# Kernel tuning notes

Hardware: AMD Instinct MI355X
Metric: run time of the kernel (lower is better)

## Reference

```python
import jax, jax.numpy as jnp
import numpy as np

B, C, H, W = 8, 256, 64, 64
CM = C // 4          # mask channels (theta/phi out) = 64
CI = C - CM          # img channels = 192
EPS = 1e-5


def setup_inputs() -> dict:
    key = jax.random.key(0)
    ks = jax.random.split(key, 12)
    return {
        "x": jax.random.normal(ks[0], (B, C, H, W), dtype=jnp.float32),
        "g_w": jax.random.normal(ks[1], (C, C), dtype=jnp.float32) * 0.05,
        "g_b": jax.random.normal(ks[2], (C,), dtype=jnp.float32) * 0.01,
        "theta_w": jax.random.normal(ks[3], (CM, CM), dtype=jnp.float32) * 0.1,
        "theta_b": jax.random.normal(ks[4], (CM,), dtype=jnp.float32) * 0.01,
        "phi_w": jax.random.normal(ks[5], (CM, CI), dtype=jnp.float32) * 0.06,
        "phi_b": jax.random.normal(ks[6], (CM,), dtype=jnp.float32) * 0.01,
        "W_w": jax.random.normal(ks[7], (C, C), dtype=jnp.float32) * 0.05,
        "W_b": jax.random.normal(ks[8], (C,), dtype=jnp.float32) * 0.01,
        "bn_gamma": jax.random.normal(ks[9], (C,), dtype=jnp.float32) * 0.1 + 1.0,
        "bn_beta": jax.random.normal(ks[10], (C,), dtype=jnp.float32) * 0.01,
        "bn_mean": jax.random.normal(ks[11], (C,), dtype=jnp.float32) * 0.1,
        "bn_var": jnp.ones((C,), dtype=jnp.float32),
    }


def _conv1x1(t, w, b):
    # [B,Cin,H,W] x [Cout,Cin] -> [B,Cout,H,W]
    return jnp.einsum('bchw,oc->bohw', t, w) + b[None, :, None, None]


def _maxpool2(t):
    b, c, h, w = t.shape
    return t.reshape(b, c, h // 2, 2, w // 2, 2).max(axis=(3, 5))


def reference(x, g_w, g_b, theta_w, theta_b, phi_w, phi_b, W_w, W_b,
              bn_gamma, bn_beta, bn_mean, bn_var):
    b, c, h, w = x.shape
    ci = c // 4
    mask_ch = x[:, :ci]          # [B, C/4, H, W]
    img_ch = x[:, ci:]           # [B, 3C/4, H, W]

    # g: conv1x1 then 2x2 maxpool -> [B, C, N'] -> [B, N', C]
    g_x = _maxpool2(_conv1x1(x, g_w, g_b)).reshape(b, c, -1).transpose(0, 2, 1)
    # theta: conv1x1 on mask -> [B, N, C/4]
    theta_x = _conv1x1(mask_ch, theta_w, theta_b).reshape(b, ci, -1).transpose(0, 2, 1)
    # phi: conv1x1 on img then pool -> [B, C/4, N']
    phi_x = _maxpool2(_conv1x1(img_ch, phi_w, phi_b)).reshape(b, ci, -1)

    f = jnp.einsum('bnc,bcm->bnm', theta_x, phi_x)     # [B, N, N']
    f_div_C = jax.nn.softmax(f, axis=-1)
    y = jnp.einsum('bnm,bmc->bnc', f_div_C, g_x)       # [B, N, C]
    y = y.transpose(0, 2, 1).reshape(b, c, h, w)

    W_y = _conv1x1(y, W_w, W_b)
    # BatchNorm (inference form with running stats)
    inv = jax.lax.rsqrt(bn_var + EPS)
    W_y = (W_y - bn_mean[None, :, None, None]) * (inv * bn_gamma)[None, :, None, None] \
          + bn_beta[None, :, None, None]
    return W_y + x
```

## Files before the change

kernel.cpp:

```cpp
#include <hip/hip_runtime.h>
#include <hip/hip_bf16.h>

typedef __hip_bfloat16 bf16;
typedef unsigned short ushort;
typedef unsigned int uint;
typedef __attribute__((ext_vector_type(8))) short short8;
typedef __attribute__((ext_vector_type(4))) float f32x4;

#define Bn 8
#define Cn 256
#define Nn 4096
#define Mn 1024
#define EPSf 1e-5f

__device__ __forceinline__ float b2f(const bf16 v){ return __bfloat162float(v); }
__device__ __forceinline__ ushort f2bu(float f){
  uint u = __float_as_uint(f);
  return (ushort)((u + 0x7FFFu + ((u >> 16) & 1u)) >> 16);
}

__global__ __launch_bounds__(256) void transpose_kernel(
    const float* __restrict__ x, bf16* __restrict__ xT)
{
  __shared__ float xs[64][65];
  const int t = threadIdx.x;
  const int p0 = blockIdx.x*64, c0 = blockIdx.y*64, b = blockIdx.z;
  #pragma unroll
  for (int i = 0; i < 16; ++i) {
    int idx = t + i*256; int cl = idx >> 6, pl = idx & 63;
    xs[cl][pl] = x[((long)(b*Cn) + c0 + cl)*Nn + p0 + pl];
  }
  __syncthreads();
  ushort* xTu = (ushort*)xT;
  #pragma unroll
  for (int i = 0; i < 8; ++i) {
    int idx = t + i*256; int pl = idx >> 5, cp = idx & 31;
    uint u = (uint)f2bu(xs[cp*2][pl]) | ((uint)f2bu(xs[cp*2+1][pl]) << 16);
    *(uint*)(xTu + ((long)(b*Nn) + p0 + pl)*Cn + c0 + cp*2) = u;
  }
}

__global__ __launch_bounds__(256) void wcomb_kernel(
    const float* __restrict__ tw, const float* __restrict__ tb,
    const float* __restrict__ pw, const float* __restrict__ pb,
    const float* __restrict__ gw, const float* __restrict__ gb,
    bf16* __restrict__ Wcomb, float* __restrict__ bcomb)
{
  const int r = blockIdx.x, c = threadIdx.x;
  float v;
  if (r < 64)        v = (c < 64)  ? tw[r*64 + c]            : 0.f;
  else if (r < 128)  v = (c >= 64) ? pw[(r-64)*192 + (c-64)] : 0.f;
  else               v = gw[(r-128)*256 + c];
  Wcomb[r*256 + c] = __float2bfloat16(v);
  if (c == 0)
    bcomb[r] = (r < 64) ? tb[r] : (r < 128) ? pb[r-64] : gb[r-128];
}

__global__ __launch_bounds__(256) void gemm384_kernel(
    const bf16* __restrict__ xT, const bf16* __restrict__ Wcomb,
    const float* __restrict__ bcomb, bf16* __restrict__ Q,
    bf16* __restrict__ K, bf16* __restrict__ Vt)
{
  __shared__ union {
    struct { ushort As[128*40]; ushort Bs[128*40]; } g;
    float Pb[2][128][33];
  } sm;
  const int t = threadIdx.x;
  const int px = blockIdx.x, o0 = blockIdx.y*128, b = blockIdx.z;
  const int p0 = px*128;
  const int lane = t & 63, w = t >> 6;
  const int ql = lane & 15, quad = lane >> 4;
  const int wm = (w & 1)*64, wn = (w >> 1)*64;
  const ushort* xTu = (const ushort*)xT;
  const ushort* Wu  = (const ushort*)Wcomb;

  f32x4 acc[4][4];
  #pragma unroll
  for (int i = 0; i < 4; ++i)
    #pragma unroll
    for (int j = 0; j < 4; ++j) acc[i][j] = (f32x4){0.f,0.f,0.f,0.f};

  for (int kc = 0; kc < 8; ++kc) {
    __syncthreads();
    #pragma unroll
    for (int i = 0; i < 2; ++i) {
      int idx = t + i*256; int r = idx >> 2, cq = idx & 3;
      *(uint4*)(sm.g.As + r*40 + cq*8) =
          *(const uint4*)(xTu + ((long)(b*Nn) + p0 + r)*Cn + kc*32 + cq*8);
      *(uint4*)(sm.g.Bs + r*40 + cq*8) =
          *(const uint4*)(Wu + (o0 + r)*Cn + kc*32 + cq*8);
    }
    __syncthreads();
    short8 aF[4], bF[4];
    #pragma unroll
    for (int mi = 0; mi < 4; ++mi)
      aF[mi] = *(const short8*)(sm.g.As + (wm + mi*16 + ql)*40 + quad*8);
    #pragma unroll
    for (int ni = 0; ni < 4; ++ni)
      bF[ni] = *(const short8*)(sm.g.Bs + (wn + ni*16 + ql)*40 + quad*8);
    #pragma unroll
    for (int mi = 0; mi < 4; ++mi)
      #pragma unroll
      for (int ni = 0; ni < 4; ++ni)
        acc[mi][ni] = __builtin_amdgcn_mfma_f32_16x16x32_bf16(aF[mi], bF[ni], acc[mi][ni], 0, 0, 0);
  }
  float bias[4];
  #pragma unroll
  for (int ni = 0; ni < 4; ++ni) bias[ni] = bcomb[o0 + wn + ni*16 + ql];

  if (o0 == 0 && wn == 0) {
    #pragma unroll
    for (int mi = 0; mi < 4; ++mi)
      #pragma unroll
      for (int ni = 0; ni < 4; ++ni)
        #pragma unroll
        for (int r = 0; r < 4; ++r) {
          int p = p0 + wm + mi*16 + quad*4 + r;
          Q[((long)(b*Nn) + p)*64 + ni*16 + ql] = __float2bfloat16(acc[mi][ni][r] + bias[ni]);
        }
  }
  __syncthreads();
  if (o0 != 0 || wn == 64) {
    int g = w & 1;
    #pragma unroll
    for (int mi = 0; mi < 4; ++mi)
      #pragma unroll
      for (int ni = 0; ni < 4; ++ni) {
        float a0 = acc[mi][ni][0] + bias[ni], a1 = acc[mi][ni][1] + bias[ni];
        float a2 = acc[mi][ni][2] + bias[ni], a3 = acc[mi][ni][3] + bias[ni];
        int o = wn + ni*16 + ql;
        int wp = mi*8 + quad*2;
        sm.Pb[g][o][wp]     = fmaxf(a0, a1);
        sm.Pb[g][o][wp + 1] = fmaxf(a2, a3);
      }
  }
  __syncthreads();
  if (o0 == 0) {
    int wp = t & 31, og = t >> 5;
    ushort kv[8];
    #pragma unroll
    for (int j = 0; j < 8; ++j) {
      int o = 64 + og*8 + j;
      kv[j] = f2bu(fmaxf(sm.Pb[0][o][wp], sm.Pb[1][o][wp]));
    }
    *(uint4*)((ushort*)K + ((long)(b*Mn) + px*32 + wp)*64 + og*8) = *(uint4*)kv;
  } else {
    int ol = t >> 1, wp0 = (t & 1)*16;
    ushort vv[16];
    #pragma unroll
    for (int j = 0; j < 16; ++j)
      vv[j] = f2bu(fmaxf(sm.Pb[0][ol][wp0 + j], sm.Pb[1][ol][wp0 + j]));
    ushort* dst = (ushort*)Vt + ((long)(b*Cn) + (o0 - 128) + ol)*Mn + px*32 + wp0;
    *(uint4*)dst       = *(uint4*)(vv);
    *(uint4*)(dst + 8) = *(uint4*)(vv + 8);
  }
}

__global__ __launch_bounds__(256) void attn_kernel(
    const bf16* __restrict__ Q, const bf16* __restrict__ K, const bf16* __restrict__ Vt,
    bf16* __restrict__ Y)
{
  __shared__ __align__(16) ushort Ks[64*72];
  __shared__ __align__(16) ushort Vs[256*72];
  __shared__ __align__(16) ushort Ps[64*72];
  __shared__ float a_sh[64];
  __shared__ float l_sh[64];

  const int t = threadIdx.x;
  const int b = blockIdx.y, q0 = blockIdx.x*64;
  const int lane = t & 63, w = t >> 6;
  const int ql = lane & 15, quad = lane >> 4;
  const int rql = w*16;
  const int pvr = (w & 1)*32;
  const int pvc = (w >> 1)*128;
  const ushort* Qu = (const ushort*)Q;
  const ushort* Ku = (const ushort*)K;
  const ushort* Vu = (const ushort*)Vt;

  short8 aQ0 = *(const short8*)(Qu + ((long)(b*Nn) + q0 + rql + ql)*64 + quad*8);
  short8 aQ1 = *(const short8*)(Qu + ((long)(b*Nn) + q0 + rql + ql)*64 + 32 + quad*8);

  float mrow[4], lrow[4];
  #pragma unroll
  for (int r = 0; r < 4; ++r) { mrow[r] = -3e38f; lrow[r] = 0.f; }

  f32x4 acc[2][8];
  #pragma unroll
  for (int mi = 0; mi < 2; ++mi)
    #pragma unroll
    for (int ci = 0; ci < 8; ++ci) acc[mi][ci] = (f32x4){0.f,0.f,0.f,0.f};

  for (int mt = 0; mt < 16; ++mt) {
    const int m0 = mt*64;
    __syncthreads();
    {
      int ch = t & 7, rr = t >> 3;
      #pragma unroll
      for (int i = 0; i < 2; ++i) {
        int row = rr + 32*i;
        *(uint4*)(Ks + row*72 + ch*8) =
            *(const uint4*)(Ku + ((long)(b*Mn) + m0 + row)*64 + ch*8);
      }
      #pragma unroll
      for (int p = 0; p < 8; ++p) {
        int n = rr + 32*p;
        *(uint4*)(Vs + n*72 + ch*8) =
            *(const uint4*)(Vu + ((long)(b*Cn) + n)*Mn + m0 + ch*8);
      }
    }
    __syncthreads();
    f32x4 s[4];
    #pragma unroll
    for (int ct = 0; ct < 4; ++ct) {
      short8 b0 = *(const short8*)(Ks + (ct*16 + ql)*72 + quad*8);
      short8 b1 = *(const short8*)(Ks + (ct*16 + ql)*72 + 32 + quad*8);
      s[ct] = (f32x4){0.f,0.f,0.f,0.f};
      s[ct] = __builtin_amdgcn_mfma_f32_16x16x32_bf16(aQ0, b0, s[ct], 0, 0, 0);
      s[ct] = __builtin_amdgcn_mfma_f32_16x16x32_bf16(aQ1, b1, s[ct], 0, 0, 0);
    }
    float alpha[4];
    #pragma unroll
    for (int r = 0; r < 4; ++r) {
      float mx = fmaxf(fmaxf(s[0][r], s[1][r]), fmaxf(s[2][r], s[3][r]));
      #pragma unroll
      for (int off = 1; off < 16; off <<= 1) mx = fmaxf(mx, __shfl_xor(mx, off, 64));
      float mn = fmaxf(mrow[r], mx);
      alpha[r] = __expf(mrow[r] - mn);
      mrow[r] = mn;
      float sum = 0.f;
      #pragma unroll
      for (int ct = 0; ct < 4; ++ct) { s[ct][r] = __expf(s[ct][r] - mn); sum += s[ct][r]; }
      #pragma unroll
      for (int off = 1; off < 16; off <<= 1) sum += __shfl_xor(sum, off, 64);
      lrow[r] = lrow[r]*alpha[r] + sum;
    }
    #pragma unroll
    for (int ct = 0; ct < 4; ++ct)
      #pragma unroll
      for (int r = 0; r < 4; ++r)
        Ps[(rql + quad*4 + r)*72 + ct*16 + ql] = f2bu(s[ct][r]);
    if (ql == 0) {
      #pragma unroll
      for (int r = 0; r < 4; ++r) a_sh[rql + quad*4 + r] = alpha[r];
    }
    __syncthreads();
    #pragma unroll
    for (int mi = 0; mi < 2; ++mi) {
      #pragma unroll
      for (int r = 0; r < 4; ++r) {
        float alv = a_sh[pvr + mi*16 + quad*4 + r];
        #pragma unroll
        for (int ci = 0; ci < 8; ++ci) acc[mi][ci][r] *= alv;
      }
    }
    short8 aP0[2], aP1[2];
    #pragma unroll
    for (int mi = 0; mi < 2; ++mi) {
      aP0[mi] = *(const short8*)(Ps + (pvr + mi*16 + ql)*72 + quad*8);
      aP1[mi] = *(const short8*)(Ps + (pvr + mi*16 + ql)*72 + 32 + quad*8);
    }
    #pragma unroll
    for (int ci = 0; ci < 8; ++ci) {
      short8 b0 = *(const short8*)(Vs + (pvc + ci*16 + ql)*72 + quad*8);
      short8 b1 = *(const short8*)(Vs + (pvc + ci*16 + ql)*72 + 32 + quad*8);
      #pragma unroll
      for (int mi = 0; mi < 2; ++mi) {
        acc[mi][ci] = __builtin_amdgcn_mfma_f32_16x16x32_bf16(aP0[mi], b0, acc[mi][ci], 0, 0, 0);
        acc[mi][ci] = __builtin_amdgcn_mfma_f32_16x16x32_bf16(aP1[mi], b1, acc[mi][ci], 0, 0, 0);
      }
    }
  }
  if (ql == 0) {
    #pragma unroll
    for (int r = 0; r < 4; ++r) l_sh[rql + quad*4 + r] = lrow[r];
  }
  __syncthreads();
  #pragma unroll
  for (int mi = 0; mi < 2; ++mi)
    #pragma unroll
    for (int r = 0; r < 4; ++r) {
      int row = pvr + mi*16 + quad*4 + r;
      float inv = 1.f / l_sh[row];
      #pragma unroll
      for (int ci = 0; ci < 8; ++ci)
        Y[((long)(b*Nn) + q0 + row)*256 + pvc + ci*16 + ql] = __float2bfloat16(acc[mi][ci][r]*inv);
    }
}

__global__ __launch_bounds__(256) void wconv_kernel(
    const bf16* __restrict__ Y, const float* __restrict__ Ww, const float* __restrict__ Wb,
    const float* __restrict__ gamma, const float* __restrict__ beta,
    const float* __restrict__ mean, const float* __restrict__ var,
    const float* __restrict__ x, float* __restrict__ out)
{
  __shared__ __align__(16) ushort As[128*40];
  __shared__ __align__(16) ushort Bs[128*40];
  __shared__ float ssc[128], ssh[128];
  const int t = threadIdx.x;
  const int n0 = blockIdx.x*128, o0 = blockIdx.y*128, b = blockIdx.z;
  const int lane = t & 63, w = t >> 6;
  const int ql = lane & 15, quad = lane >> 4;
  const int wm = (w & 1)*64, wn = (w >> 1)*64;
  const ushort* Yu = (const ushort*)Y;

  if (t < 128) {
    int o = o0 + t;
    float sc = gamma[o] * rsqrtf(var[o] + EPSf);
    ssc[t] = sc;
    ssh[t] = (Wb[o] - mean[o])*sc + beta[o];
  }

  f32x4 acc[4][4];
  #pragma unroll
  for (int i = 0; i < 4; ++i)
    #pragma unroll
    for (int j = 0; j < 4; ++j) acc[i][j] = (f32x4){0.f,0.f,0.f,0.f};

  for (int kc = 0; kc < 8; ++kc) {
    __syncthreads();
    #pragma unroll
    for (int i = 0; i < 4; ++i) {
      int idx = t + i*256; int r = idx >> 3, cq = idx & 7;
      float4 v = *(const float4*)(Ww + (o0 + r)*Cn + kc*32 + cq*4);
      uint lo = (uint)f2bu(v.x) | ((uint)f2bu(v.y) << 16);
      uint hi = (uint)f2bu(v.z) | ((uint)f2bu(v.w) << 16);
      *(uint2*)(As + r*40 + cq*4) = make_uint2(lo, hi);
    }
    #pragma unroll
    for (int i = 0; i < 2; ++i) {
      int idx = t + i*256; int r = idx >> 2, cq = idx & 3;
      *(uint4*)(Bs + r*40 + cq*8) =
          *(const uint4*)(Yu + ((long)(b*Nn) + n0 + r)*Cn + kc*32 + cq*8);
    }
    __syncthreads();
    short8 aF[4], bF[4];
    #pragma unroll
    for (int mi = 0; mi < 4; ++mi)
      aF[mi] = *(const short8*)(As + (wm + mi*16 + ql)*40 + quad*8);
    #pragma unroll
    for (int ni = 0; ni < 4; ++ni)
      bF[ni] = *(const short8*)(Bs + (wn + ni*16 + ql)*40 + quad*8);
    #pragma unroll
    for (int mi = 0; mi < 4; ++mi)
      #pragma unroll
      for (int ni = 0; ni < 4; ++ni)
        acc[mi][ni] = __builtin_amdgcn_mfma_f32_16x16x32_bf16(aF[mi], bF[ni], acc[mi][ni], 0, 0, 0);
  }
  #pragma unroll
  for (int mi = 0; mi < 4; ++mi)
    #pragma unroll
    for (int r = 0; r < 4; ++r) {
      int ol = wm + mi*16 + quad*4 + r;
      int o = o0 + ol;
      float sc = ssc[ol], sh = ssh[ol];
      #pragma unroll
      for (int ni = 0; ni < 4; ++ni) {
        int n = n0 + wn + ni*16 + ql;
        long gidx = ((long)(b*Cn + o))*Nn + n;
        out[gidx] = acc[mi][ni][r]*sc + sh + x[gidx];
      }
    }
}

extern "C" void kernel_launch(void* const* d_in, const int* in_sizes, int n_in,
                              void* d_out, int out_size, void* d_ws, size_t ws_size,
                              hipStream_t stream)
{
  const float* x       = (const float*)d_in[0];
  const float* g_w     = (const float*)d_in[1];
  const float* g_b     = (const float*)d_in[2];
  const float* theta_w = (const float*)d_in[3];
  const float* theta_b = (const float*)d_in[4];
  const float* phi_w   = (const float*)d_in[5];
  const float* phi_b   = (const float*)d_in[6];
  const float* W_w     = (const float*)d_in[7];
  const float* W_b     = (const float*)d_in[8];
  const float* bn_g    = (const float*)d_in[9];
  const float* bn_b    = (const float*)d_in[10];
  const float* bn_m    = (const float*)d_in[11];
  const float* bn_v    = (const float*)d_in[12];
  float* out = (float*)d_out;

  bf16* wsb = (bf16*)d_ws;
  bf16* xT    = wsb;
  bf16* Y     = wsb;
  bf16* Q     = wsb + 8388608;
  bf16* K     = wsb + 10485760;
  bf16* Vt    = wsb + 11010048;
  bf16* Wcomb = wsb + 13107200;
  float* bcomb = (float*)(wsb + 13205504);

  transpose_kernel<<<dim3(64, 4, Bn), 256, 0, stream>>>(x, xT);
  wcomb_kernel<<<dim3(384), 256, 0, stream>>>(theta_w, theta_b, phi_w, phi_b, g_w, g_b, Wcomb, bcomb);
  gemm384_kernel<<<dim3(32, 3, Bn), 256, 0, stream>>>(xT, Wcomb, bcomb, Q, K, Vt);
  attn_kernel<<<dim3(64, Bn), 256, 0, stream>>>(Q, K, Vt, Y);
  wconv_kernel<<<dim3(32, 2, Bn), 256, 0, stream>>>(Y, W_w, W_b, bn_g, bn_b, bn_m, bn_v, x, out);
}
```

Baseline: 201.9 us.

## Precompute softmax row max in a first pass and drop online rescaling

The attention kernel now runs an extra pass over all K tiles, read straight from global memory, to compute the exact row maximum before the main loop. The main loop then drops the per-tile max reduction, the alpha rescaling of the accumulators and the a_sh shared array, and only accumulates unnormalised exp sums, which are reduced once at the end. The LDS row pitch also shrinks from 72 to 68 elements. That pitch gives 136-byte rows, so the 16-byte LDS vector accesses are no longer 16-byte aligned, which may split or slow them. The extra pass also recomputes the QK products once more.

Measured after the change: 216.6 us. 7.3% more time.

```diff
diff --git a/kernel.cpp b/kernel.cpp
--- a/kernel.cpp
+++ b/kernel.cpp
@@ -160,10 +160,9 @@
     const bf16* __restrict__ Q, const bf16* __restrict__ K, const bf16* __restrict__ Vt,
     bf16* __restrict__ Y)
 {
-  __shared__ __align__(16) ushort Ks[64*72];
-  __shared__ __align__(16) ushort Vs[256*72];
-  __shared__ __align__(16) ushort Ps[64*72];
-  __shared__ float a_sh[64];
+  __shared__ __align__(16) ushort Ks[64*68];
+  __shared__ __align__(16) ushort Vs[256*68];
+  __shared__ __align__(16) ushort Ps[64*68];
   __shared__ float l_sh[64];
 
   const int t = threadIdx.x;
@@ -177,12 +176,35 @@
   const ushort* Ku = (const ushort*)K;
   const ushort* Vu = (const ushort*)Vt;
 
-  short8 aQ0 = *(const short8*)(Qu + ((long)(b*Nn) + q0 + rql + ql)*64 + quad*8);
-  short8 aQ1 = *(const short8*)(Qu + ((long)(b*Nn) + q0 + rql + ql)*64 + 32 + quad*8);
-
-  float mrow[4], lrow[4];
-  #pragma unroll
-  for (int r = 0; r < 4; ++r) { mrow[r] = -3e38f; lrow[r] = 0.f; }
+  const long qrow = (long)(b*Nn) + q0 + rql + ql;
+  short8 aQ0 = *(const short8*)(Qu + qrow*64 + quad*8);
+  short8 aQ1 = *(const short8*)(Qu + qrow*64 + 32 + quad*8);
+
+  float mrow[4];
+  #pragma unroll
+  for (int r = 0; r < 4; ++r) mrow[r] = -3e38f;
+  for (int mt = 0; mt < 16; ++mt) {
+    const ushort* kb = Ku + ((long)(b*Mn) + mt*64)*64;
+    #pragma unroll
+    for (int ct = 0; ct < 4; ++ct) {
+      short8 b0 = *(const short8*)(kb + (ct*16 + ql)*64 + quad*8);
+      short8 b1 = *(const short8*)(kb + (ct*16 + ql)*64 + 32 + quad*8);
+      f32x4 s = (f32x4){0.f,0.f,0.f,0.f};
+      s = __builtin_amdgcn_mfma_f32_16x16x32_bf16(aQ0, b0, s, 0, 0, 0);
+      s = __builtin_amdgcn_mfma_f32_16x16x32_bf16(aQ1, b1, s, 0, 0, 0);
+      #pragma unroll
+      for (int r = 0; r < 4; ++r) mrow[r] = fmaxf(mrow[r], s[r]);
+    }
+  }
+  #pragma unroll
+  for (int r = 0; r < 4; ++r)
+    #pragma unroll
+    for (int off = 1; off < 16; off <<= 1)
+      mrow[r] = fmaxf(mrow[r], __shfl_xor(mrow[r], off, 64));
+
+  float lrow[4];
+  #pragma unroll
+  for (int r = 0; r < 4; ++r) lrow[r] = 0.f;
 
   f32x4 acc[2][8];
   #pragma unroll
@@ -198,13 +220,13 @@
       #pragma unroll
       for (int i = 0; i < 2; ++i) {
         int row = rr + 32*i;
-        *(uint4*)(Ks + row*72 + ch*8) =
+        *(uint4*)(Ks + row*68 + ch*8) =
             *(const uint4*)(Ku + ((long)(b*Mn) + m0 + row)*64 + ch*8);
       }
       #pragma unroll
       for (int p = 0; p < 8; ++p) {
         int n = rr + 32*p;
-        *(uint4*)(Vs + n*72 + ch*8) =
+        *(uint4*)(Vs + n*68 + ch*8) =
             *(const uint4*)(Vu + ((long)(b*Cn) + n)*Mn + m0 + ch*8);
       }
     }
@@ -212,57 +234,31 @@
     f32x4 s[4];
     #pragma unroll
     for (int ct = 0; ct < 4; ++ct) {
-      short8 b0 = *(const short8*)(Ks + (ct*16 + ql)*72 + quad*8);
-      short8 b1 = *(const short8*)(Ks + (ct*16 + ql)*72 + 32 + quad*8);
+      short8 b0 = *(const short8*)(Ks + (ct*16 + ql)*68 + quad*8);
+      short8 b1 = *(const short8*)(Ks + (ct*16 + ql)*68 + 32 + quad*8);
       s[ct] = (f32x4){0.f,0.f,0.f,0.f};
       s[ct] = __builtin_amdgcn_mfma_f32_16x16x32_bf16(aQ0, b0, s[ct], 0, 0, 0);
       s[ct] = __builtin_amdgcn_mfma_f32_16x16x32_bf16(aQ1, b1, s[ct], 0, 0, 0);
     }
-    float alpha[4];
-    #pragma unroll
-    for (int r = 0; r < 4; ++r) {
-      float mx = fmaxf(fmaxf(s[0][r], s[1][r]), fmaxf(s[2][r], s[3][r]));
-      #pragma unroll
-      for (int off = 1; off < 16; off <<= 1) mx = fmaxf(mx, __shfl_xor(mx, off, 64));
-      float mn = fmaxf(mrow[r], mx);
-      alpha[r] = __expf(mrow[r] - mn);
-      mrow[r] = mn;
-      float sum = 0.f;
-      #pragma unroll
-      for (int ct = 0; ct < 4; ++ct) { s[ct][r] = __expf(s[ct][r] - mn); sum += s[ct][r]; }
-      #pragma unroll
-      for (int off = 1; off < 16; off <<= 1) sum += __shfl_xor(sum, off, 64);
-      lrow[r] = lrow[r]*alpha[r] + sum;
-    }
     #pragma unroll
     for (int ct = 0; ct < 4; ++ct)
       #pragma unroll
-      for (int r = 0; r < 4; ++r)
-        Ps[(rql + quad*4 + r)*72 + ct*16 + ql] = f2bu(s[ct][r]);
-    if (ql == 0) {
-      #pragma unroll
-      for (int r = 0; r < 4; ++r) a_sh[rql + quad*4 + r] = alpha[r];
-    }
-    __syncthreads();
+      for (int r = 0; r < 4; ++r) {
+        float e = __expf(s[ct][r] - mrow[r]);
+        lrow[r] += e;
+        Ps[(rql + quad*4 + r)*68 + ct*16 + ql] = f2bu(e);
+      }
+    __syncthreads();
+    short8 aP0[2], aP1[2];
     #pragma unroll
     for (int mi = 0; mi < 2; ++mi) {
-      #pragma unroll
-      for (int r = 0; r < 4; ++r) {
-        float alv = a_sh[pvr + mi*16 + quad*4 + r];
-        #pragma unroll
-        for (int ci = 0; ci < 8; ++ci) acc[mi][ci][r] *= alv;
-      }
-    }
-    short8 aP0[2], aP1[2];
-    #pragma unroll
-    for (int mi = 0; mi < 2; ++mi) {
-      aP0[mi] = *(const short8*)(Ps + (pvr + mi*16 + ql)*72 + quad*8);
-      aP1[mi] = *(const short8*)(Ps + (pvr + mi*16 + ql)*72 + 32 + quad*8);
+      aP0[mi] = *(const short8*)(Ps + (pvr + mi*16 + ql)*68 + quad*8);
+      aP1[mi] = *(const short8*)(Ps + (pvr + mi*16 + ql)*68 + 32 + quad*8);
     }
     #pragma unroll
     for (int ci = 0; ci < 8; ++ci) {
-      short8 b0 = *(const short8*)(Vs + (pvc + ci*16 + ql)*72 + quad*8);
-      short8 b1 = *(const short8*)(Vs + (pvc + ci*16 + ql)*72 + 32 + quad*8);
+      short8 b0 = *(const short8*)(Vs + (pvc + ci*16 + ql)*68 + quad*8);
+      short8 b1 = *(const short8*)(Vs + (pvc + ci*16 + ql)*68 + 32 + quad*8);
       #pragma unroll
       for (int mi = 0; mi < 2; ++mi) {
         acc[mi][ci] = __builtin_amdgcn_mfma_f32_16x16x32_bf16(aP0[mi], b0, acc[mi][ci], 0, 0, 0);
@@ -270,6 +266,11 @@
       }
     }
   }
+  #pragma unroll
+  for (int r = 0; r < 4; ++r)
+    #pragma unroll
+    for (int off = 1; off < 16; off <<= 1)
+      lrow[r] += __shfl_xor(lrow[r], off, 64);
   if (ql == 0) {
     #pragma unroll
     for (int r = 0; r < 4; ++r) l_sh[rql + quad*4 + r] = lrow[r];
```
